# Kernel tuning notes

Hardware: AMD Instinct MI355X
Metric: run time of the kernel (lower is better)

## Reference

```python
import jax, jax.numpy as jnp
import numpy as np

DIM = 2048
HEADS = 16
HEAD_DIM = DIM // HEADS
EPS = 1e-5


def layernorm(x, g, b):
    mu = jnp.mean(x, axis=-1, keepdims=True)
    var = jnp.mean(jnp.square(x - mu), axis=-1, keepdims=True)
    return (x - mu) * jax.lax.rsqrt(var + EPS) * g + b


def bitlinear(x, w):
    # BitNet b1.58: per-tensor ternary weight quant + per-token int8 absmax activation quant
    ws = jnp.clip(jnp.mean(jnp.abs(w)), 1e-5, None)          # weight scale (mean |w|)
    wq = jnp.clip(jnp.round(w / ws), -1.0, 1.0) * ws          # ternary {-1,0,1}*ws
    xs = 127.0 / jnp.clip(jnp.max(jnp.abs(x), axis=-1, keepdims=True), 1e-5, None)
    xq = jnp.clip(jnp.round(x * xs), -128.0, 127.0) / xs      # int8 absmax, dequantized
    return jnp.einsum('bnc,oc->bno', xq, wq)


def attention(x, w_qkv, w_proj):
    B, N, C = x.shape
    qkv = bitlinear(x, w_qkv).reshape(B, N, 3, HEADS, HEAD_DIM)
    q, k, v = [qkv[:, :, i].transpose(0, 2, 1, 3) for i in range(3)]  # [B,H,N,D]
    scores = jnp.einsum('bhqd,bhkd->bhqk', q, k) / jnp.sqrt(jnp.asarray(HEAD_DIM, x.dtype))
    attn = jax.nn.softmax(scores, axis=-1)
    o = jnp.einsum('bhqk,bhkd->bhqd', attn, v)
    o = o.transpose(0, 2, 1, 3).reshape(B, N, C)
    return bitlinear(o, w_proj)


def setup_inputs() -> dict:
    key = jax.random.key(0)
    ks = jax.random.split(key, 9)
    s = 0.02
    return {
        'x': jax.random.normal(ks[0], (2, 2048, DIM), dtype=jnp.float32),
        'w_qkv': jax.random.normal(ks[1], (3 * DIM, DIM), dtype=jnp.float32) * s,
        'w_proj': jax.random.normal(ks[2], (DIM, DIM), dtype=jnp.float32) * s,
        'w_fc1': jax.random.normal(ks[3], (4 * DIM, DIM), dtype=jnp.float32) * s,
        'w_fc2': jax.random.normal(ks[4], (DIM, 4 * DIM), dtype=jnp.float32) * s,
        'g1': jnp.ones((DIM,), jnp.float32),
        'b1': jnp.zeros((DIM,), jnp.float32),
        'g2': jnp.ones((DIM,), jnp.float32),
        'b2': jnp.zeros((DIM,), jnp.float32),
    }


def reference(x, w_qkv, w_proj, w_fc1, w_fc2, g1, b1, g2, b2):
    x = x + attention(layernorm(x, g1, b1), w_qkv, w_proj)
    h = bitlinear(layernorm(x, g2, b2), w_fc1)
    h = jax.nn.gelu(h, approximate=False)
    h = bitlinear(h, w_fc2)
    return x + h
```

## Files before the change

### kernel.cpp

```cpp
#include <hip/hip_runtime.h>
#include <cstdint>

#define DEVI __device__ __forceinline__

typedef int v4i __attribute__((ext_vector_type(4)));
typedef short v8s __attribute__((ext_vector_type(8)));
typedef float v4f __attribute__((ext_vector_type(4)));

DEVI float bf_lo(unsigned u) { return __uint_as_float(u << 16); }
DEVI float bf_hi(unsigned u) { return __uint_as_float(u & 0xffff0000u); }
DEVI float bf2f(unsigned short h) { return __uint_as_float(((unsigned)h) << 16); }
DEVI unsigned short f2bf(float f) {
  unsigned u = __float_as_uint(f);
  u += 0x7fffu + ((u >> 16) & 1u);
  return (unsigned short)(u >> 16);
}

DEVI void async_copy16(void* l, const void* g) {
  __builtin_amdgcn_global_load_lds((const __attribute__((address_space(1))) void*)g,
                                   (__attribute__((address_space(3))) void*)l,
                                   16, 0, 0);
}

DEVI float wave_sum(float v) {
#pragma unroll
  for (int o = 32; o > 0; o >>= 1) v += __shfl_xor(v, o, 64);
  return v;
}
DEVI float wave_max(float v) {
#pragma unroll
  for (int o = 32; o > 0; o >>= 1) v = fmaxf(v, __shfl_xor(v, o, 64));
  return v;
}

__global__ __launch_bounds__(256) void absum4_kernel(const float* __restrict__ w0,
                                                     const float* __restrict__ w1,
                                                     const float* __restrict__ w2,
                                                     const float* __restrict__ w3,
                                                     float* __restrict__ acc) {
  int t = blockIdx.x & 3;
  int bid = blockIdx.x >> 2;
  int nb = gridDim.x >> 2;
  const float* w = t == 0 ? w0 : t == 1 ? w1 : t == 2 ? w2 : w3;
  long n = t == 0 ? 12582912L : t == 1 ? 4194304L : 16777216L;
  long stride = (long)nb * 1024;
  float s = 0.f;
  for (long i = ((long)bid * 256 + threadIdx.x) * 4; i < n; i += stride) {
    float4 v = *(const float4*)(w + i);
    s += fabsf(v.x) + fabsf(v.y) + fabsf(v.z) + fabsf(v.w);
  }
  s = wave_sum(s);
  __shared__ float sc[4];
  int tid = threadIdx.x;
  if ((tid & 63) == 0) sc[tid >> 6] = s;
  __syncthreads();
  if (tid == 0) atomicAdd(acc + t, sc[0] + sc[1] + sc[2] + sc[3]);
}

__global__ __launch_bounds__(256) void wquant4_kernel(const float* __restrict__ w0,
                                                      const float* __restrict__ w1,
                                                      const float* __restrict__ w2,
                                                      const float* __restrict__ w3,
                                                      const float* __restrict__ acc,
                                                      signed char* __restrict__ o0,
                                                      signed char* __restrict__ o1,
                                                      signed char* __restrict__ o2,
                                                      signed char* __restrict__ o3) {
  int t = blockIdx.x & 3;
  int bid = blockIdx.x >> 2;
  int nb = gridDim.x >> 2;
  const float* w;
  signed char* out;
  long n4;
  float cnt;
  int kshift;
  if (t == 0)      { w = w0; out = o0; n4 = 3145728L; cnt = 12582912.f; kshift = 11; }
  else if (t == 1) { w = w1; out = o1; n4 = 1048576L; cnt = 4194304.f;  kshift = 11; }
  else if (t == 2) { w = w2; out = o2; n4 = 4194304L; cnt = 16777216.f; kshift = 11; }
  else             { w = w3; out = o3; n4 = 4194304L; cnt = 16777216.f; kshift = 13; }
  float wsv = fmaxf(acc[t] / cnt, 1e-5f);
  float inv = 1.0f / wsv;
  int K = 1 << kshift;
  long stride = (long)nb * 256;
  for (long i = (long)bid * 256 + threadIdx.x; i < n4; i += stride) {
    float4 v = *(const float4*)(w + i * 4);
    int q0 = max(-1, min(1, (int)rintf(v.x * inv)));
    int q1 = max(-1, min(1, (int)rintf(v.y * inv)));
    int q2 = max(-1, min(1, (int)rintf(v.z * inv)));
    int q3 = max(-1, min(1, (int)rintf(v.w * inv)));
    unsigned r = (q0 & 0xff) | ((q1 & 0xff) << 8) | ((q2 & 0xff) << 16) | ((q3 & 0xff) << 24);
    long flat = i * 4;
    int n = (int)(flat >> kshift);
    int k = (int)(flat & (K - 1));
    long off = ((long)(n >> 4) * (K >> 6) + (k >> 6)) * 1024 +
               (((k >> 4) & 3) * 16 + (n & 15)) * 16 + (k & 15);
    *(unsigned*)(out + off) = r;
  }
}

__global__ __launch_bounds__(256) void ln_quant_kernel(const float* __restrict__ x,
                                                       const float* __restrict__ g,
                                                       const float* __restrict__ b,
                                                       signed char* __restrict__ q,
                                                       float* __restrict__ inv_s) {
  int row = blockIdx.x, tid = threadIdx.x;
  const float4* xr = (const float4*)(x + (long)row * 2048);
  float4 a0 = xr[tid * 2], a1 = xr[tid * 2 + 1];
  float xv[8] = {a0.x, a0.y, a0.z, a0.w, a1.x, a1.y, a1.z, a1.w};
  float s = 0.f, s2 = 0.f;
#pragma unroll
  for (int e = 0; e < 8; ++e) { s += xv[e]; s2 += xv[e] * xv[e]; }
  s = wave_sum(s); s2 = wave_sum(s2);
  __shared__ float sc[8];
  if ((tid & 63) == 0) { sc[tid >> 6] = s; sc[4 + (tid >> 6)] = s2; }
  __syncthreads();
  float mean = (sc[0] + sc[1] + sc[2] + sc[3]) * (1.f / 2048.f);
  float var = (sc[4] + sc[5] + sc[6] + sc[7]) * (1.f / 2048.f) - mean * mean;
  float rs = 1.0f / sqrtf(var + 1e-5f);
  float4 g0 = ((const float4*)g)[tid * 2], g1v = ((const float4*)g)[tid * 2 + 1];
  float4 b0 = ((const float4*)b)[tid * 2], b1v = ((const float4*)b)[tid * 2 + 1];
  float gv[8] = {g0.x, g0.y, g0.z, g0.w, g1v.x, g1v.y, g1v.z, g1v.w};
  float bv[8] = {b0.x, b0.y, b0.z, b0.w, b1v.x, b1v.y, b1v.z, b1v.w};
  float y[8];
  float am = 0.f;
#pragma unroll
  for (int e = 0; e < 8; ++e) {
    y[e] = (xv[e] - mean) * rs * gv[e] + bv[e];
    am = fmaxf(am, fabsf(y[e]));
  }
  am = wave_max(am);
  __syncthreads();
  if ((tid & 63) == 0) sc[tid >> 6] = am;
  __syncthreads();
  am = fmaxf(fmaxf(sc[0], sc[1]), fmaxf(sc[2], sc[3]));
  float c = fmaxf(am, 1e-5f);
  float xs = 127.0f / c;
  union { signed char c8[8]; int2 v; } u;
#pragma unroll
  for (int e = 0; e < 8; ++e) {
    int t = (int)rintf(y[e] * xs);
    u.c8[e] = (signed char)max(-128, min(127, t));
  }
  ((int2*)(q + (long)row * 2048))[tid] = u.v;
  if (tid == 0) inv_s[row] = c * (1.0f / 127.0f);
}

template <int R>
__global__ __launch_bounds__(256) void row_quant_kernel(const unsigned short* __restrict__ in,
                                                        signed char* __restrict__ q,
                                                        float* __restrict__ inv_s) {
  constexpr int V = R / 2048;
  int row = blockIdx.x, tid = threadIdx.x;
  const uint4* p = (const uint4*)(in + (long)row * R);
  float y[V * 8];
  float am = 0.f;
#pragma unroll
  for (int v = 0; v < V; ++v) {
    uint4 d = p[tid * V + v];
    unsigned xw[4] = {d.x, d.y, d.z, d.w};
#pragma unroll
    for (int k = 0; k < 4; ++k) {
      y[v * 8 + k * 2] = bf_lo(xw[k]);
      y[v * 8 + k * 2 + 1] = bf_hi(xw[k]);
    }
  }
#pragma unroll
  for (int e = 0; e < V * 8; ++e) am = fmaxf(am, fabsf(y[e]));
  am = wave_max(am);
  __shared__ float sc[4];
  if ((tid & 63) == 0) sc[tid >> 6] = am;
  __syncthreads();
  am = fmaxf(fmaxf(sc[0], sc[1]), fmaxf(sc[2], sc[3]));
  float c = fmaxf(am, 1e-5f);
  float xs = 127.0f / c;
  signed char* qr = q + (long)row * R;
#pragma unroll
  for (int v = 0; v < V; ++v) {
    union { signed char c8[8]; long l; } u;
#pragma unroll
    for (int k = 0; k < 8; ++k) {
      int t = (int)rintf(y[v * 8 + k] * xs);
      u.c8[k] = (signed char)max(-128, min(127, t));
    }
    ((long*)qr)[tid * V + v] = u.l;
  }
  if (tid == 0) inv_s[row] = c * (1.0f / 127.0f);
}

template <int EPI>
__global__ __launch_bounds__(256)
void gemm_i8(const signed char* __restrict__ A, const signed char* __restrict__ Bp,
             int N, int K, const float* __restrict__ wacc, float wcount,
             const float* __restrict__ inv_s, const float* __restrict__ res,
             void* __restrict__ outp) {
  __shared__ signed char As[2][128 * 128];
  int tid = threadIdx.x;
  int idx = blockIdx.x;
  int r8 = idx & 7, rest = idx >> 3;
  int mb = rest & 31;
  int nb = (rest >> 5) * 8 + r8;
  int m0 = mb * 128, n0 = nb * 128;
  int w = tid >> 6, lane = tid & 63;
  int wm = (w >> 1) * 64, wn = (w & 1) * 64;
  int lr = lane & 15, q = lane >> 4;

  v4i acc[4][4] = {};

  int srow = w * 32 + (lane >> 3);
  int scol = (lane & 7) ^ ((lane >> 3) & 7);
  const signed char* ga = A + (long)(m0 + srow) * K + scol * 16;

  int nkb = K >> 7;
  const signed char* gbp[4];
#pragma unroll
  for (int t = 0; t < 4; ++t) {
    int ntile = (n0 >> 4) + (w & 1) * 4 + t;
    gbp[t] = Bp + (long)ntile * (K >> 6) * 1024 + lane * 16;
  }

  v4i bf_cur[2][4], bf_nxt[2][4];
#pragma unroll
  for (int i = 0; i < 4; ++i)
    async_copy16(&As[0][(w * 256 + i * 64) * 16], ga + i * 8 * K);
#pragma unroll
  for (int s = 0; s < 2; ++s)
#pragma unroll
    for (int t = 0; t < 4; ++t) bf_cur[s][t] = *(const v4i*)(gbp[t] + s * 1024);
  __syncthreads();

  int buf = 0;
  for (int kb = 0; kb < nkb; ++kb) {
    if (kb + 1 < nkb) {
#pragma unroll
      for (int i = 0; i < 4; ++i)
        async_copy16(&As[buf ^ 1][(w * 256 + i * 64) * 16], ga + i * 8 * K + (kb + 1) * 128);
#pragma unroll
      for (int s = 0; s < 2; ++s)
#pragma unroll
        for (int t = 0; t < 4; ++t)
          bf_nxt[s][t] = *(const v4i*)(gbp[t] + ((kb + 1) * 2 + s) * 1024);
    }
#pragma unroll
    for (int s = 0; s < 2; ++s) {
      v4i af[4];
#pragma unroll
      for (int i = 0; i < 4; ++i) {
        int row = wm + i * 16 + lr;
        af[i] = *(const v4i*)(&As[buf][(row * 8 + ((s * 4 + q) ^ (lr & 7))) * 16]);
      }
#pragma unroll
      for (int i = 0; i < 4; ++i)
#pragma unroll
        for (int j = 0; j < 4; ++j)
          acc[i][j] = __builtin_amdgcn_mfma_i32_16x16x64_i8(af[i], bf_cur[s][j], acc[i][j], 0, 0, 0);
    }
    __syncthreads();
    if (kb + 1 < nkb) {
#pragma unroll
      for (int s = 0; s < 2; ++s)
#pragma unroll
        for (int t = 0; t < 4; ++t) bf_cur[s][t] = bf_nxt[s][t];
    }
    buf ^= 1;
  }

  float wsv = fmaxf(wacc[0] / wcount, 1e-5f);
#pragma unroll
  for (int i = 0; i < 4; ++i) {
    int rowbase = m0 + wm + i * 16 + (lane >> 4) * 4;
#pragma unroll
    for (int r = 0; r < 4; ++r) {
      int row = rowbase + r;
      float s = wsv * inv_s[row];
#pragma unroll
      for (int j = 0; j < 4; ++j) {
        int col = n0 + wn + j * 16 + (lane & 15);
        long off = (long)row * N + col;
        float v = (float)acc[i][j][r] * s;
        if constexpr (EPI == 0) {
          ((unsigned short*)outp)[off] = f2bf(v);
        } else if constexpr (EPI == 1) {
          ((float*)outp)[off] = v + res[off];
        } else {
          float gvv = 0.5f * v * (1.0f + erff(v * 0.70710678118654752f));
          ((unsigned short*)outp)[off] = f2bf(gvv);
        }
      }
    }
  }
}

#define GIB_DS(AF, MLO, RBUF)                                                           \
  _Pragma("unroll") for (int j = 0; j < 4; ++j) {                                       \
    int m = (MLO) + (j >> 1), kc = j & 1;                                               \
    int row = wm + m * 16 + lr;                                                         \
    AF[j] = *(const v4i*)(&As[(RBUF)][(row * 8 + ((kc * 4 + q) ^ (lr & 7))) * 16]);     \
  }

#define GIB_MM(AF, MLO, BFC)                                                            \
  _Pragma("unroll") for (int j2 = 0; j2 < 2; ++j2)                                      \
    _Pragma("unroll") for (int t = 0; t < 4; ++t)                                       \
      _Pragma("unroll") for (int kc = 0; kc < 2; ++kc)                                  \
        acc[(MLO) + j2][t] = __builtin_amdgcn_mfma_i32_16x16x64_i8(                     \
            AF[j2 * 2 + kc], BFC[kc][t], acc[(MLO) + j2][t], 0, 0, 0);

#define GIB_PH(DSISSUE, VMISSUE, WAITSTR, MMPART, TAIL)                                 \
  {                                                                                     \
    DSISSUE                                                                             \
    __builtin_amdgcn_sched_barrier(0);                                                  \
    VMISSUE                                                                             \
    __builtin_amdgcn_sched_barrier(0);                                                  \
    __builtin_amdgcn_s_barrier();                                                       \
    asm volatile(WAITSTR ::: "memory");                                                 \
    __builtin_amdgcn_sched_barrier(0);                                                  \
    __builtin_amdgcn_s_setprio(1);                                                      \
    MMPART                                                                              \
    __builtin_amdgcn_s_setprio(0);                                                      \
    __builtin_amdgcn_sched_barrier(0);                                                  \
    TAIL                                                                                \
    __builtin_amdgcn_s_barrier();                                                       \
  }

#define GIB_STAGE(RBD)                                                                  \
  _Pragma("unroll") for (int i = 0; i < 4; ++i)                                         \
    async_copy16(&As[(RBD)][(w * 256 + i * 64) * 16],                                   \
                 ga + (long)i * 8 * K + (kb + 1) * 128);

#define GIB_LOADB(DST, HALF)                                                            \
  _Pragma("unroll") for (int t = 0; t < 4; ++t)                                         \
    asm volatile("global_load_dwordx4 %0, %1, off"                                      \
                 : "=v"(DST[HALF][t])                                                   \
                 : "v"(gbp[t] + (long)((kb + 1) * 2 + (HALF)) * 1024)                   \
                 : "memory");

#define GIB_VMTAIL                                                                      \
  asm volatile("s_waitcnt vmcnt(8)" ::: "memory");                                      \
  __builtin_amdgcn_sched_barrier(0);

#define GIB_ITER_MAIN(RB, BFC, BFN)                                                     \
  {                                                                                     \
    GIB_PH(GIB_DS(afA, 0, RB) GIB_DS(afB, 2, RB), GIB_STAGE((RB) ^ 1),                  \
           "s_waitcnt vmcnt(4) lgkmcnt(4)", GIB_MM(afA, 0, BFC), )                      \
    GIB_PH(GIB_DS(afA, 4, RB), GIB_LOADB(BFN, 0),                                       \
           "s_waitcnt lgkmcnt(4)", GIB_MM(afB, 2, BFC), )                               \
    GIB_PH(GIB_DS(afB, 6, RB), GIB_LOADB(BFN, 1),                                       \
           "s_waitcnt lgkmcnt(4)", GIB_MM(afA, 4, BFC), )                               \
    GIB_PH(, , "s_waitcnt lgkmcnt(0)", GIB_MM(afB, 6, BFC), GIB_VMTAIL)                 \
  }

#define GIB_ITER_LAST(RB, BFC)                                                          \
  {                                                                                     \
    GIB_PH(GIB_DS(afA, 0, RB) GIB_DS(afB, 2, RB), ,                                     \
           "s_waitcnt vmcnt(0) lgkmcnt(4)", GIB_MM(afA, 0, BFC), )                      \
    GIB_PH(GIB_DS(afA, 4, RB), , "s_waitcnt lgkmcnt(4)", GIB_MM(afB, 2, BFC), )         \
    GIB_PH(GIB_DS(afB, 6, RB), , "s_waitcnt lgkmcnt(4)", GIB_MM(afA, 4, BFC), )         \
    GIB_PH(, , "s_waitcnt lgkmcnt(0)", GIB_MM(afB, 6, BFC), )                           \
  }

template <int EPI>
__global__ __launch_bounds__(512, 2)
void gemm_i8_big(const signed char* __restrict__ A, const signed char* __restrict__ Bp,
                 int N, int K, const float* __restrict__ wacc, float wcount,
                 const float* __restrict__ inv_s, const float* __restrict__ res,
                 void* __restrict__ outp) {
  __shared__ signed char As[2][256 * 128];
  int tid = threadIdx.x;
  int idx = blockIdx.x;
  int r8 = idx & 7, rest = idx >> 3;
  int mb = rest & 15;
  int nb = (rest >> 4) * 8 + r8;
  int m0 = mb * 256, n0 = nb * 256;
  int w = tid >> 6, lane = tid & 63;
  int wm = (w >> 2) * 128, wn = (w & 3) * 64;
  int lr = lane & 15, q = lane >> 4;

  v4i acc[8][4] = {};

  int srow = w * 32 + (lane >> 3);
  int scol = (lane & 7) ^ ((lane >> 3) & 7);
  const signed char* ga = A + (long)(m0 + srow) * K + scol * 16;

  int nkt = K >> 7;
  const signed char* gbp[4];
#pragma unroll
  for (int t = 0; t < 4; ++t) {
    int ntile = ((n0 + wn) >> 4) + t;
    gbp[t] = Bp + (long)ntile * (K >> 6) * 1024 + lane * 16;
  }

  v4i bfA[2][4], bfB[2][4];
  v4i afA[4], afB[4];
#pragma unroll
  for (int i = 0; i < 4; ++i)
    async_copy16(&As[0][(w * 256 + i * 64) * 16], ga + (long)i * 8 * K);
  __builtin_amdgcn_sched_barrier(0);
#pragma unroll
  for (int s = 0; s < 2; ++s)
#pragma unroll
    for (int t = 0; t < 4; ++t)
      asm volatile("global_load_dwordx4 %0, %1, off"
                   : "=v"(bfA[s][t]) : "v"(gbp[t] + (long)s * 1024) : "memory");
  __builtin_amdgcn_sched_barrier(0);
  asm volatile("s_waitcnt vmcnt(8)" ::: "memory");
  __builtin_amdgcn_sched_barrier(0);
  __builtin_amdgcn_s_barrier();

  for (int kb2 = 0; kb2 < nkt - 2; kb2 += 2) {
    { int kb = kb2;     GIB_ITER_MAIN(0, bfA, bfB) }
    { int kb = kb2 + 1; GIB_ITER_MAIN(1, bfB, bfA) }
  }
  { int kb = nkt - 2; GIB_ITER_MAIN(0, bfA, bfB) }
  GIB_ITER_LAST(1, bfB)

  float wsv = fmaxf(wacc[0] / wcount, 1e-5f);
#pragma unroll
  for (int m = 0; m < 8; ++m) {
    int rowbase = m0 + wm + m * 16 + q * 4;
#pragma unroll
    for (int r = 0; r < 4; ++r) {
      int row = rowbase + r;
      float s = wsv * inv_s[row];
#pragma unroll
      for (int j = 0; j < 4; ++j) {
        int col = n0 + wn + j * 16 + lr;
        long off = (long)row * N + col;
        float v = (float)acc[m][j][r] * s;
        if constexpr (EPI == 0) {
          ((unsigned short*)outp)[off] = f2bf(v);
        } else if constexpr (EPI == 1) {
          ((float*)outp)[off] = v + res[off];
        } else {
          float gvv = 0.5f * v * (1.0f + erff(v * 0.70710678118654752f));
          ((unsigned short*)outp)[off] = f2bf(gvv);
        }
      }
    }
  }
}

DEVI int sigma_k(int y) {
  return (y & 35) | (((y >> 3) & 1) << 4) | (((y >> 2) & 1) << 3) | (((y >> 4) & 1) << 2);
}

DEVI void stage_k(const unsigned short* kbase_g, int k0, char* ks, int w, int lane) {
#pragma unroll
  for (int i = 0; i < 2; ++i) {
    int c = i * 512 + w * 64 + lane;
    int key = c >> 4;
    int dch = (c & 15) ^ (key & 15);
    async_copy16(ks + (i * 512 + w * 64) * 16,
                 kbase_g + (long)(k0 + sigma_k(key)) * 6144 + dch * 8);
  }
}

DEVI void load_v(const unsigned short* vbase_g, int k0, int kg, int dg, uint2* lv) {
#pragma unroll
  for (int i = 0; i < 4; ++i)
    lv[i] = *(const uint2*)(vbase_g + (long)(k0 + kg * 4 + i) * 6144 + dg * 4);
}

DEVI void repack_v(const uint2* lv, unsigned short* vt, int kg, int dg) {
#pragma unroll
  for (int jd = 0; jd < 4; ++jd) {
    union { unsigned short s[4]; unsigned long long u; } pk;
#pragma unroll
    for (int i = 0; i < 4; ++i) {
      unsigned word = (jd < 2) ? lv[i].x : lv[i].y;
      pk.s[i] = (unsigned short)((jd & 1) ? (word >> 16) : (word & 0xffffu));
    }
    *(unsigned long long*)(vt + (dg * 4 + jd) * 72 + kg * 4) = pk.u;
  }
}

__global__ __launch_bounds__(512, 4)
void fattn_kernel(const unsigned short* __restrict__ qkv, unsigned short* __restrict__ out) {
  constexpr int VROW = 72;
  __shared__ __align__(16) char Ks[2][16384];
  __shared__ __align__(16) unsigned short Vt[2][128 * VROW];

  int tid = threadIdx.x;
  int w = tid >> 6, lane = tid & 63;
  int l = lane & 15, q = lane >> 4;
  int idx = blockIdx.x;
  int r8 = idx & 7, rest = idx >> 3;
  int qt = rest & 15;
  int bh = (rest >> 4) * 8 + r8;
  int bb = bh >> 4, hh = bh & 15;
  const unsigned short* base = qkv + (long)bb * 2048 * 6144;
  int q0 = qt * 128;

  v8s aq[4];
  {
    const unsigned short* qrow = base + (long)(q0 + w * 16 + l) * 6144 + hh * 128;
#pragma unroll
    for (int kf = 0; kf < 4; ++kf) aq[kf] = *(const v8s*)(qrow + kf * 32 + q * 8);
  }

  v4f oacc[8] = {};
  float mrow = -1e30f, lrow = 0.f;

  const unsigned short* kbase_g = base + 2048 + hh * 128;
  const unsigned short* vbase_g = base + 4096 + hh * 128;
  int kg = tid & 15, dg = tid >> 4;
  constexpr float SC = 0.08838834764831845f;

  stage_k(kbase_g, 0, Ks[0], w, lane);
  uint2 lv[4];
  load_v(vbase_g, 0, kg, dg, lv);
  repack_v(lv, Vt[0], kg, dg);
  __syncthreads();

  for (int kt = 0; kt < 32; ++kt) {
    const char* ksc = Ks[kt & 1];
    const unsigned short* vtc = Vt[kt & 1];
    bool more = kt < 31;
    if (more) {
      stage_k(kbase_g, (kt + 1) * 64, Ks[(kt + 1) & 1], w, lane);
      load_v(vbase_g, (kt + 1) * 64, kg, dg, lv);
    }

    v4f sacc[4] = {};
#pragma unroll
    for (int kf = 0; kf < 4; ++kf) {
#pragma unroll
      for (int t = 0; t < 4; ++t) {
        int ch = (t * 16 + l) * 16 + ((kf * 4 + q) ^ l);
        v8s bk = *(const v8s*)(ksc + ch * 16);
        sacc[t] = __builtin_amdgcn_mfma_f32_16x16x32_bf16(bk, aq[kf], sacc[t], 0, 0, 0);
      }
    }

    float rm = -1e30f;
#pragma unroll
    for (int t = 0; t < 4; ++t)
#pragma unroll
      for (int r = 0; r < 4; ++r) rm = fmaxf(rm, sacc[t][r]);
    rm *= SC;
    rm = fmaxf(rm, __shfl_xor(rm, 16, 64));
    rm = fmaxf(rm, __shfl_xor(rm, 32, 64));
    float mnew = fmaxf(mrow, rm);
    if (__any(mnew - mrow > 8.0f)) {
      float alpha = __expf(mrow - mnew);
      mrow = mnew;
      lrow *= alpha;
#pragma unroll
      for (int r = 0; r < 4; ++r) {
        float ao = __shfl(alpha, q * 4 + r, 64);
#pragma unroll
        for (int t = 0; t < 8; ++t) oacc[t][r] *= ao;
      }
    }
    float rs = 0.f;
#pragma unroll
    for (int t = 0; t < 4; ++t)
#pragma unroll
      for (int r = 0; r < 4; ++r) {
        float pv = __expf(fmaf(sacc[t][r], SC, -mrow));
        sacc[t][r] = pv;
        rs += pv;
      }
    rs += __shfl_xor(rs, 16, 64);
    rs += __shfl_xor(rs, 32, 64);
    lrow += rs;

    union { unsigned u[4]; v8s s; } pa[2];
#pragma unroll
    for (int s2 = 0; s2 < 2; ++s2)
#pragma unroll
      for (int j2 = 0; j2 < 4; ++j2) {
        int tt = s2 * 2 + (j2 >> 1);
        int r0 = (j2 & 1) * 2;
        unsigned wrd;
        asm("v_cvt_pk_bf16_f32 %0, %1, %2"
            : "=v"(wrd) : "v"(sacc[tt][r0]), "v"(sacc[tt][r0 + 1]));
        pa[s2].u[j2] = wrd;
      }

#pragma unroll
    for (int s2 = 0; s2 < 2; ++s2) {
#pragma unroll
      for (int t = 0; t < 8; ++t) {
        v8s bv = *(const v8s*)(vtc + (t * 16 + l) * VROW + s2 * 32 + q * 8);
        oacc[t] = __builtin_amdgcn_mfma_f32_16x16x32_bf16(pa[s2].s, bv, oacc[t], 0, 0, 0);
      }
    }

    if (more) repack_v(lv, Vt[(kt + 1) & 1], kg, dg);
    __syncthreads();
  }

#pragma unroll
  for (int r = 0; r < 4; ++r) {
    float lr = __shfl(lrow, q * 4 + r, 64);
    float inv = 1.0f / lr;
    long grow = (long)bb * 2048 + q0 + w * 16 + q * 4 + r;
    unsigned short* orow = out + grow * 2048 + hh * 128;
#pragma unroll
    for (int t = 0; t < 8; ++t) orow[t * 16 + l] = f2bf(oacc[t][r] * inv);
  }
}

extern "C" void kernel_launch(void* const* d_in, const int* in_sizes, int n_in,
                              void* d_out, int out_size, void* d_ws, size_t ws_size,
                              hipStream_t stream) {
  (void)in_sizes; (void)n_in; (void)out_size; (void)ws_size;
  const float* x      = (const float*)d_in[0];
  const float* w_qkv  = (const float*)d_in[1];
  const float* w_proj = (const float*)d_in[2];
  const float* w_fc1  = (const float*)d_in[3];
  const float* w_fc2  = (const float*)d_in[4];
  const float* g1 = (const float*)d_in[5];
  const float* b1 = (const float*)d_in[6];
  const float* g2 = (const float*)d_in[7];
  const float* b2 = (const float*)d_in[8];

  char* wsb = (char*)d_ws;
  float* acc = (float*)wsb;
  size_t off = 256;
  signed char* q8 = (signed char*)(wsb + off);       off += (size_t)4096 * 8192;
  float* invs = (float*)(wsb + off);                 off += 16384;
  signed char* wq_qkv = (signed char*)(wsb + off);   off += (size_t)6144 * 2048;
  signed char* wq_proj = (signed char*)(wsb + off);  off += (size_t)2048 * 2048;
  signed char* wq_fc1 = (signed char*)(wsb + off);   off += (size_t)8192 * 2048;
  signed char* wq_fc2 = (signed char*)(wsb + off);   off += (size_t)2048 * 8192;
  unsigned short* qkvh = (unsigned short*)(wsb + off); off += (size_t)4096 * 8192 * 2;
  unsigned short* obuf = (unsigned short*)(wsb + off); off += (size_t)4096 * 2048 * 2;
  float* x2 = (float*)(wsb + off);                   off += (size_t)4096 * 2048 * 4;

  hipMemsetAsync(acc, 0, 256, stream);

  absum4_kernel<<<4096, 256, 0, stream>>>(w_qkv, w_proj, w_fc1, w_fc2, acc);
  wquant4_kernel<<<4096, 256, 0, stream>>>(w_qkv, w_proj, w_fc1, w_fc2, acc,
                                           wq_qkv, wq_proj, wq_fc1, wq_fc2);

  ln_quant_kernel<<<4096, 256, 0, stream>>>(x, g1, b1, q8, invs);
  gemm_i8_big<0><<<16 * 24, 512, 0, stream>>>(q8, wq_qkv, 6144, 2048, acc + 0, 12582912.f, invs, nullptr, qkvh);
  fattn_kernel<<<512, 512, 0, stream>>>(qkvh, obuf);
  row_quant_kernel<2048><<<4096, 256, 0, stream>>>(obuf, q8, invs);
  gemm_i8<1><<<16 * 32, 256, 0, stream>>>(q8, wq_proj, 2048, 2048, acc + 1, 4194304.f, invs, x, x2);
  ln_quant_kernel<<<4096, 256, 0, stream>>>(x2, g2, b2, q8, invs);
  gemm_i8_big<2><<<16 * 32, 512, 0, stream>>>(q8, wq_fc1, 8192, 2048, acc + 2, 16777216.f, invs, nullptr, qkvh);
  row_quant_kernel<8192><<<4096, 256, 0, stream>>>(qkvh, q8, invs);
  gemm_i8<1><<<16 * 32, 256, 0, stream>>>(q8, wq_fc2, 2048, 8192, acc + 3, 16777216.f, invs, x2, (float*)d_out);
}
```

Baseline: 763.9 us.

## Use polynomial erf GELU, simplify GEMM phase LDS loads, raise attention MFMA priority

Measured after the change: 723.0 us. 1.06x faster.

```diff
diff --git a/kernel.cpp b/kernel.cpp
--- a/kernel.cpp
+++ b/kernel.cpp
@@ -14,6 +14,20 @@
   unsigned u = __float_as_uint(f);
   u += 0x7fffu + ((u >> 16) & 1u);
   return (unsigned short)(u >> 16);
+}
+
+DEVI float fast_gelu(float v) {
+  float xx = v * 0.70710678118654752f;
+  float ax = fabsf(xx);
+  float t = __builtin_amdgcn_rcpf(1.0f + 0.3275911f * ax);
+  float p = t * (0.254829592f +
+           t * (-0.284496736f +
+           t * (1.421413741f +
+           t * (-1.453152027f + t * 1.061405429f))));
+  float e = __expf(-ax * ax);
+  float er = 1.0f - p * e;
+  er = copysignf(er, xx);
+  return 0.5f * v * (1.0f + er);
 }
 
 DEVI void async_copy16(void* l, const void* g) {
@@ -282,31 +296,21 @@
         } else if constexpr (EPI == 1) {
           ((float*)outp)[off] = v + res[off];
         } else {
-          float gvv = 0.5f * v * (1.0f + erff(v * 0.70710678118654752f));
-          ((unsigned short*)outp)[off] = f2bf(gvv);
+          ((unsigned short*)outp)[off] = f2bf(fast_gelu(v));
         }
       }
     }
   }
 }
 
-#define GIB_DS(AF, MLO, RBUF)                                                           \
-  _Pragma("unroll") for (int j = 0; j < 4; ++j) {                                       \
-    int m = (MLO) + (j >> 1), kc = j & 1;                                               \
-    int row = wm + m * 16 + lr;                                                         \
-    AF[j] = *(const v4i*)(&As[(RBUF)][(row * 8 + ((kc * 4 + q) ^ (lr & 7))) * 16]);     \
-  }
-
-#define GIB_MM(AF, MLO, BFC)                                                            \
-  _Pragma("unroll") for (int j2 = 0; j2 < 2; ++j2)                                      \
-    _Pragma("unroll") for (int t = 0; t < 4; ++t)                                       \
-      _Pragma("unroll") for (int kc = 0; kc < 2; ++kc)                                  \
-        acc[(MLO) + j2][t] = __builtin_amdgcn_mfma_i32_16x16x64_i8(                     \
-            AF[j2 * 2 + kc], BFC[kc][t], acc[(MLO) + j2][t], 0, 0, 0);
-
-#define GIB_PH(DSISSUE, VMISSUE, WAITSTR, MMPART, TAIL)                                 \
+#define GIB_PHASE(RB, BFC, VMISSUE, WAITSTR, TAIL)                                      \
   {                                                                                     \
-    DSISSUE                                                                             \
+    v4i af[4];                                                                          \
+    _Pragma("unroll") for (int j = 0; j < 4; ++j) {                                     \
+      int m = 2 * p + (j >> 1), kc = j & 1;                                             \
+      int row = wm + m * 16 + lr;                                                       \
+      af[j] = *(const v4i*)(&As[(RB)][(row * 8 + ((kc * 4 + q) ^ (lr & 7))) * 16]);     \
+    }                                                                                   \
     __builtin_amdgcn_sched_barrier(0);                                                  \
     VMISSUE                                                                             \
     __builtin_amdgcn_sched_barrier(0);                                                  \
@@ -314,7 +318,11 @@
     asm volatile(WAITSTR ::: "memory");                                                 \
     __builtin_amdgcn_sched_barrier(0);                                                  \
     __builtin_amdgcn_s_setprio(1);                                                      \
-    MMPART                                                                              \
+    _Pragma("unroll") for (int j = 0; j < 2; ++j)                                       \
+      _Pragma("unroll") for (int t = 0; t < 4; ++t)                                     \
+        _Pragma("unroll") for (int kc = 0; kc < 2; ++kc)                                \
+          acc[2 * p + j][t] = __builtin_amdgcn_mfma_i32_16x16x64_i8(                    \
+              af[j * 2 + kc], BFC[kc][t], acc[2 * p + j][t], 0, 0, 0);                  \
     __builtin_amdgcn_s_setprio(0);                                                      \
     __builtin_amdgcn_sched_barrier(0);                                                  \
     TAIL                                                                                \
@@ -339,22 +347,26 @@
 
 #define GIB_ITER_MAIN(RB, BFC, BFN)                                                     \
   {                                                                                     \
-    GIB_PH(GIB_DS(afA, 0, RB) GIB_DS(afB, 2, RB), GIB_STAGE((RB) ^ 1),                  \
-           "s_waitcnt vmcnt(4) lgkmcnt(4)", GIB_MM(afA, 0, BFC), )                      \
-    GIB_PH(GIB_DS(afA, 4, RB), GIB_LOADB(BFN, 0),                                       \
-           "s_waitcnt lgkmcnt(4)", GIB_MM(afB, 2, BFC), )                               \
-    GIB_PH(GIB_DS(afB, 6, RB), GIB_LOADB(BFN, 1),                                       \
-           "s_waitcnt lgkmcnt(4)", GIB_MM(afA, 4, BFC), )                               \
-    GIB_PH(, , "s_waitcnt lgkmcnt(0)", GIB_MM(afB, 6, BFC), GIB_VMTAIL)                 \
+    { constexpr int p = 0;                                                              \
+      GIB_PHASE(RB, BFC, GIB_STAGE((RB) ^ 1), "s_waitcnt vmcnt(4) lgkmcnt(0)", ) }      \
+    { constexpr int p = 1;                                                              \
+      GIB_PHASE(RB, BFC, GIB_LOADB(BFN, 0), "s_waitcnt lgkmcnt(0)", ) }                 \
+    { constexpr int p = 2;                                                              \
+      GIB_PHASE(RB, BFC, GIB_LOADB(BFN, 1), "s_waitcnt lgkmcnt(0)", ) }                 \
+    { constexpr int p = 3;                                                              \
+      GIB_PHASE(RB, BFC, , "s_waitcnt lgkmcnt(0)", GIB_VMTAIL) }                        \
   }
 
 #define GIB_ITER_LAST(RB, BFC)                                                          \
   {                                                                                     \
-    GIB_PH(GIB_DS(afA, 0, RB) GIB_DS(afB, 2, RB), ,                                     \
-           "s_waitcnt vmcnt(0) lgkmcnt(4)", GIB_MM(afA, 0, BFC), )                      \
-    GIB_PH(GIB_DS(afA, 4, RB), , "s_waitcnt lgkmcnt(4)", GIB_MM(afB, 2, BFC), )         \
-    GIB_PH(GIB_DS(afB, 6, RB), , "s_waitcnt lgkmcnt(4)", GIB_MM(afA, 4, BFC), )         \
-    GIB_PH(, , "s_waitcnt lgkmcnt(0)", GIB_MM(afB, 6, BFC), )                           \
+    { constexpr int p = 0;                                                              \
+      GIB_PHASE(RB, BFC, , "s_waitcnt vmcnt(0) lgkmcnt(0)", ) }                         \
+    { constexpr int p = 1;                                                              \
+      GIB_PHASE(RB, BFC, , "s_waitcnt lgkmcnt(0)", ) }                                  \
+    { constexpr int p = 2;                                                              \
+      GIB_PHASE(RB, BFC, , "s_waitcnt lgkmcnt(0)", ) }                                  \
+    { constexpr int p = 3;                                                              \
+      GIB_PHASE(RB, BFC, , "s_waitcnt lgkmcnt(0)", ) }                                  \
   }
 
 template <int EPI>
@@ -389,7 +401,6 @@
   }
 
   v4i bfA[2][4], bfB[2][4];
-  v4i afA[4], afB[4];
 #pragma unroll
   for (int i = 0; i < 4; ++i)
     async_copy16(&As[0][(w * 256 + i * 64) * 16], ga + (long)i * 8 * K);
@@ -430,8 +441,7 @@
         } else if constexpr (EPI == 1) {
           ((float*)outp)[off] = v + res[off];
         } else {
-          float gvv = 0.5f * v * (1.0f + erff(v * 0.70710678118654752f));
-          ((unsigned short*)outp)[off] = f2bf(gvv);
+          ((unsigned short*)outp)[off] = f2bf(fast_gelu(v));
         }
       }
     }
@@ -520,6 +530,7 @@
     }
 
     v4f sacc[4] = {};
+    __builtin_amdgcn_s_setprio(1);
 #pragma unroll
     for (int kf = 0; kf < 4; ++kf) {
 #pragma unroll
@@ -529,6 +540,7 @@
         sacc[t] = __builtin_amdgcn_mfma_f32_16x16x32_bf16(bk, aq[kf], sacc[t], 0, 0, 0);
       }
     }
+    __builtin_amdgcn_s_setprio(0);
 
     float rm = -1e30f;
 #pragma unroll
@@ -576,6 +588,7 @@
         pa[s2].u[j2] = wrd;
       }
 
+    __builtin_amdgcn_s_setprio(1);
 #pragma unroll
     for (int s2 = 0; s2 < 2; ++s2) {
 #pragma unroll
@@ -584,6 +597,7 @@
         oacc[t] = __builtin_amdgcn_mfma_f32_16x16x32_bf16(pa[s2].s, bv, oacc[t], 0, 0, 0);
       }
     }
+    __builtin_amdgcn_s_setprio(0);
 
     if (more) repack_v(lv, Vt[(kt + 1) & 1], kg, dg);
     __syncthreads();
```
